# Kernel optimization log

Hardware: AMD Instinct MI355X
Metric: run time of the kernel (lower is better)

Reference implementation:

```python
import jax, jax.numpy as jnp
import numpy as np

DEPTH = 11          # tree depth
D = 1024            # input_width
H = 32              # hidden_width (leaf MLP)
O = 1024            # output_width
B = 4096            # flattened token batch
N_LEAVES = 2 ** DEPTH
N_NODES = 2 ** DEPTH - 1


def setup_inputs() -> dict:
    key = jax.random.key(0)
    ks = jax.random.split(key, 7)
    f1 = 1.0 / np.sqrt(D)
    f2 = 1.0 / np.sqrt(H)
    u = lambda k, shape, f: jax.random.uniform(k, shape, jnp.float32, -f, f)
    return {
        "x": jax.random.normal(ks[0], (B, D), jnp.float32),
        "node_weights": u(ks[1], (N_NODES, D), f1),
        "node_biases": u(ks[2], (N_NODES,), f1),   # (n_nodes,1) in torch; flattened
        "w1s": u(ks[3], (N_LEAVES, D, H), f1),
        "b1s": u(ks[4], (N_LEAVES, H), f1),
        "w2s": u(ks[5], (N_LEAVES, H, O), f2),
        "b2s": u(ks[6], (N_LEAVES, O), f2),
    }


def reference(x, node_weights, node_biases, w1s, b1s, w2s, b2s):
    # --- hard tree descent (eval_forward) ---
    nodes = jnp.zeros((x.shape[0],), jnp.int32)
    for i in range(DEPTH):  # fixed small loop over tree depth
        w = node_weights[nodes]                       # [B, D] gathered plane coeffs
        b = node_biases[nodes]                        # [B]
        score = jnp.einsum('bd,bd->b', x, w) + b      # per-sample dot product
        choice = (score >= 0).astype(jnp.int32)
        platform = 2 ** i - 1
        next_platform = 2 ** (i + 1) - 1
        nodes = (nodes - platform) * 2 + choice + next_platform
    leaves = nodes - (2 ** DEPTH - 1)                 # [B] leaf index per sample

    # --- per-sample leaf MLP with gathered weights ---
    h = jax.nn.relu(jnp.einsum('bd,bdh->bh', x, w1s[leaves]) + b1s[leaves])  # [B, H]
    out = jnp.einsum('bh,bho->bo', h, w2s[leaves]) + b2s[leaves]             # [B, O]
    return out
```

## Files before the change

kernel.cpp:

```cpp
#include <hip/hip_runtime.h>

#define DEPTH 11
#define D 1024
#define H 32
#define OW 1024
#define B 4096
#define N_LEAVES 2048
#define N_NODES 2047
#define SMAX 4
#define MAX_ITEMS 3072

typedef __attribute__((address_space(3))) void lds_void;
typedef const __attribute__((address_space(1))) void glb_void;

#define WAITV8  do { asm volatile("s_waitcnt vmcnt(8)" ::: "memory"); __builtin_amdgcn_sched_barrier(0); } while (0)
#define WAITV4  do { asm volatile("s_waitcnt vmcnt(4)" ::: "memory"); __builtin_amdgcn_sched_barrier(0); } while (0)
#define WAITV0  do { asm volatile("s_waitcnt vmcnt(0)" ::: "memory"); __builtin_amdgcn_sched_barrier(0); } while (0)
#define WAITLG0 do { asm volatile("s_waitcnt lgkmcnt(0)" ::: "memory"); __builtin_amdgcn_sched_barrier(0); } while (0)

__global__ __launch_bounds__(256) void descent_kernel(
    const float* __restrict__ x, const float* __restrict__ nw,
    const float* __restrict__ nb, int* __restrict__ leaf,
    int* __restrict__ rnk, int* __restrict__ count)
{
    int lane = threadIdx.x & 63;
    int wv   = threadIdx.x >> 6;
    int samp = blockIdx.x * 4 + wv;

    const float4* xp = (const float4*)(x + (size_t)samp * D);
    float4 xf[4];
#pragma unroll
    for (int k = 0; k < 4; k++) xf[k] = xp[lane + 64 * k];

    int node = 0;
#pragma unroll
    for (int i = 0; i < DEPTH; i++) {
        const float4* wp = (const float4*)(nw + (size_t)node * D);
        double s = 0.0;
#pragma unroll
        for (int k = 0; k < 4; k++) {
            float4 wf = wp[lane + 64 * k];
            s += (double)xf[k].x * (double)wf.x;
            s += (double)xf[k].y * (double)wf.y;
            s += (double)xf[k].z * (double)wf.z;
            s += (double)xf[k].w * (double)wf.w;
        }
#pragma unroll
        for (int m = 32; m >= 1; m >>= 1) s += __shfl_xor(s, m, 64);
        double score = s + (double)nb[node];
        int choice = (score >= 0.0) ? 1 : 0;
        node = 2 * node + 1 + choice;
    }
    int lf = node - N_NODES;
    if (lane == 0) {
        leaf[samp] = lf;
        rnk[samp]  = atomicAdd(&count[lf], 1);
    }
}

__global__ __launch_bounds__(256) void scan_kernel(
    const int* __restrict__ count, int* __restrict__ offsets)
{
    __shared__ int tot[256];
    int t = threadIdx.x;
    int c[8], s = 0;
#pragma unroll
    for (int k = 0; k < 8; k++) { c[k] = count[t * 8 + k]; s += c[k]; }
    tot[t] = s;
    __syncthreads();
    for (int off = 1; off < 256; off <<= 1) {
        int v = (t >= off) ? tot[t - off] : 0;
        __syncthreads();
        tot[t] += v;
        __syncthreads();
    }
    int base = (t > 0) ? tot[t - 1] : 0;
#pragma unroll
    for (int k = 0; k < 8; k++) { offsets[t * 8 + k] = base; base += c[k]; }
}

__global__ __launch_bounds__(256) void scatter_kernel(
    const int* __restrict__ leaf, const int* __restrict__ rnk,
    const int* __restrict__ offsets, int* __restrict__ bucket)
{
    int i = blockIdx.x * 256 + threadIdx.x;
    bucket[offsets[leaf[i]] + rnk[i]] = i;
}

__global__ __launch_bounds__(256) void build_items_kernel(
    const int* __restrict__ count, int* __restrict__ items,
    int* __restrict__ nitems)
{
    int l = blockIdx.x * 256 + threadIdx.x;
    int c = count[l];
    if (c > 0) {
        int k = (c + SMAX - 1) / SMAX;
        int base = atomicAdd(nitems, k);
        for (int i = 0; i < k; i++)
            items[base + i] = l | ((i * SMAX) << 11);
    }
}

__device__ __forceinline__ void stage4k(const float* src, float* dst, int lane)
{
#pragma unroll
    for (int i = 0; i < 4; i++)
        __builtin_amdgcn_global_load_lds((glb_void*)(src + i * 256 + lane * 4),
                                         (lds_void*)(dst + i * 256), 16, 0, 0);
}

__device__ __forceinline__ void stageL2(const float* w2w, int cj, float* dst, int lane)
{
#pragma unroll
    for (int jl = 0; jl < 4; jl++)
        __builtin_amdgcn_global_load_lds(
            (glb_void*)(w2w + (size_t)(cj * 4 + jl) * OW + lane * 4),
            (lds_void*)(dst + jl * 256), 16, 0, 0);
}

template <int SS>
__device__ __forceinline__ void l1c(const float* p, const float* xsw, int c,
                                    int lane, int dg, float4* acc)
{
#pragma unroll
    for (int u = 0; u < 4; u++) {
        float4 w = ((const float4*)p)[u * 64 + lane];
#pragma unroll
        for (int s = 0; s < SS; s++) {
            float xv = xsw[s * D + c * 32 + u * 8 + dg];
            acc[s].x += xv * w.x;
            acc[s].y += xv * w.y;
            acc[s].z += xv * w.z;
            acc[s].w += xv * w.w;
        }
    }
}

template <int SS>
__device__ __forceinline__ void l2c(const float* p, const float (*hs)[H], int cj,
                                    int lane, float4* o)
{
#pragma unroll
    for (int jl = 0; jl < 4; jl++) {
        float4 w = ((const float4*)p)[jl * 64 + lane];
#pragma unroll
        for (int s = 0; s < SS; s++) {
            float hv = hs[s][cj * 4 + jl];
            o[s].x += hv * w.x;
            o[s].y += hv * w.y;
            o[s].z += hv * w.z;
            o[s].w += hv * w.w;
        }
    }
}

template <int SS>
__device__ __forceinline__ void mlp_item(
    int tid, const float* __restrict__ x, const float* __restrict__ w1,
    const float* __restrict__ w2, const float* __restrict__ b1,
    const float* __restrict__ b2, const int* __restrict__ bucket, int base,
    float* xs, float* wq, float (*pl1)[SMAX][32], float (*hs)[H],
    float* __restrict__ out)
{
    const int lane = tid & 63, wave = tid >> 6;
    const int jq = lane & 7, dg = lane >> 3;

    float b1v = b1[tid & 31];
    asm volatile("" :: "v"(b1v));

    int sid[SS];
#pragma unroll
    for (int s = 0; s < SS; s++) sid[s] = bucket[base + s];

#pragma unroll
    for (int s = 0; s < SS; s++)
        __builtin_amdgcn_global_load_lds(
            (glb_void*)(x + (size_t)sid[s] * D + wave * 256 + lane * 4),
            (lds_void*)(xs + s * D + wave * 256), 16, 0, 0);

    const float* w1w = w1 + wave * 8192;
    const float* xsw = xs + wave * 256;
    stage4k(w1w + 0 * 1024, wq + 0 * 1024, lane);
    stage4k(w1w + 1 * 1024, wq + 1 * 1024, lane);
    stage4k(w1w + 2 * 1024, wq + 2 * 1024, lane);

    float4 acc[SS];
#pragma unroll
    for (int s = 0; s < SS; s++) acc[s] = make_float4(0.f, 0.f, 0.f, 0.f);

    WAITV8; l1c<SS>(wq + 0 * 1024, xsw, 0, lane, dg, acc); stage4k(w1w + 3 * 1024, wq + 0 * 1024, lane);
    WAITV8; l1c<SS>(wq + 1 * 1024, xsw, 1, lane, dg, acc); stage4k(w1w + 4 * 1024, wq + 1 * 1024, lane);
    WAITV8; l1c<SS>(wq + 2 * 1024, xsw, 2, lane, dg, acc); stage4k(w1w + 5 * 1024, wq + 2 * 1024, lane);
    WAITV8; l1c<SS>(wq + 0 * 1024, xsw, 3, lane, dg, acc); stage4k(w1w + 6 * 1024, wq + 0 * 1024, lane);
    WAITV8; l1c<SS>(wq + 1 * 1024, xsw, 4, lane, dg, acc); stage4k(w1w + 7 * 1024, wq + 1 * 1024, lane);
    WAITV8; l1c<SS>(wq + 2 * 1024, xsw, 5, lane, dg, acc);
    WAITV4; l1c<SS>(wq + 0 * 1024, xsw, 6, lane, dg, acc);
    WAITV0; l1c<SS>(wq + 1 * 1024, xsw, 7, lane, dg, acc);

#pragma unroll
    for (int m = 8; m <= 32; m <<= 1)
#pragma unroll
        for (int s = 0; s < SS; s++) {
            acc[s].x += __shfl_xor(acc[s].x, m, 64);
            acc[s].y += __shfl_xor(acc[s].y, m, 64);
            acc[s].z += __shfl_xor(acc[s].z, m, 64);
            acc[s].w += __shfl_xor(acc[s].w, m, 64);
        }
    if (dg == 0) {
#pragma unroll
        for (int s = 0; s < SS; s++)
            *(float4*)&pl1[wave][s][jq * 4] = acc[s];
    }

    const float* w2w = w2 + wave * 256;
    stageL2(w2w, 0, wq + 0 * 1024, lane);
    stageL2(w2w, 1, wq + 1 * 1024, lane);
    stageL2(w2w, 2, wq + 2 * 1024, lane);

    WAITLG0;
    __builtin_amdgcn_s_barrier();
    if (tid < 32 * SS) {
        int s2 = tid >> 5, j2 = tid & 31;
        float sum = pl1[0][s2][j2] + pl1[1][s2][j2] + pl1[2][s2][j2] +
                    pl1[3][s2][j2] + b1v;
        hs[s2][j2] = fmaxf(sum, 0.f);
    }
    WAITLG0;
    __builtin_amdgcn_s_barrier();

    float4 o[SS];
#pragma unroll
    for (int s = 0; s < SS; s++) o[s] = make_float4(0.f, 0.f, 0.f, 0.f);

    WAITV8; l2c<SS>(wq + 0 * 1024, hs, 0, lane, o); stageL2(w2w, 3, wq + 0 * 1024, lane);
    WAITV8; l2c<SS>(wq + 1 * 1024, hs, 1, lane, o); stageL2(w2w, 4, wq + 1 * 1024, lane);
    WAITV8; l2c<SS>(wq + 2 * 1024, hs, 2, lane, o); stageL2(w2w, 5, wq + 2 * 1024, lane);
    WAITV8; l2c<SS>(wq + 0 * 1024, hs, 3, lane, o); stageL2(w2w, 6, wq + 0 * 1024, lane);
    WAITV8; l2c<SS>(wq + 1 * 1024, hs, 4, lane, o); stageL2(w2w, 7, wq + 1 * 1024, lane);
    WAITV8; l2c<SS>(wq + 2 * 1024, hs, 5, lane, o);
    WAITV4; l2c<SS>(wq + 0 * 1024, hs, 6, lane, o);
    WAITV0; l2c<SS>(wq + 1 * 1024, hs, 7, lane, o);

    float4 bv = *(const float4*)(b2 + wave * 256 + lane * 4);
#pragma unroll
    for (int s = 0; s < SS; s++) {
        float4 o4;
        o4.x = o[s].x + bv.x;
        o4.y = o[s].y + bv.y;
        o4.z = o[s].z + bv.z;
        o4.w = o[s].w + bv.w;
        *(float4*)(out + (size_t)sid[s] * OW + wave * 256 + lane * 4) = o4;
    }
}

__global__ __launch_bounds__(256, 2) void mlp_kernel(
    const float* __restrict__ x, const float* __restrict__ w1s,
    const float* __restrict__ b1s, const float* __restrict__ w2s,
    const float* __restrict__ b2s, const int* __restrict__ offsets,
    const int* __restrict__ count, const int* __restrict__ bucket,
    const int* __restrict__ items, const int* __restrict__ nitems,
    float* __restrict__ out)
{
    __shared__ float xs[SMAX * D];
    __shared__ float wbuf[4 * 3 * 1024];
    __shared__ float pl1[4][SMAX][32];
    __shared__ float hs[SMAX][H];

    if ((int)blockIdx.x >= nitems[0]) return;
    int item  = items[blockIdx.x];
    int l     = item & (N_LEAVES - 1);
    int start = item >> 11;
    int S     = min(SMAX, count[l] - start);
    int base  = offsets[l] + start;
    int tid   = threadIdx.x;

    const float* w1 = w1s + (size_t)l * D * H;
    const float* w2 = w2s + (size_t)l * H * OW;
    const float* b1 = b1s + (size_t)l * H;
    const float* b2 = b2s + (size_t)l * OW;
    float* wq = wbuf + (tid >> 6) * 3 * 1024;

    switch (S) {
        case 1: mlp_item<1>(tid, x, w1, w2, b1, b2, bucket, base, xs, wq, pl1, hs, out); break;
        case 2: mlp_item<2>(tid, x, w1, w2, b1, b2, bucket, base, xs, wq, pl1, hs, out); break;
        case 3: mlp_item<3>(tid, x, w1, w2, b1, b2, bucket, base, xs, wq, pl1, hs, out); break;
        default: mlp_item<4>(tid, x, w1, w2, b1, b2, bucket, base, xs, wq, pl1, hs, out); break;
    }
}

extern "C" void kernel_launch(void* const* d_in, const int* in_sizes, int n_in,
                              void* d_out, int out_size, void* d_ws, size_t ws_size,
                              hipStream_t stream)
{
    const float* x   = (const float*)d_in[0];
    const float* nw  = (const float*)d_in[1];
    const float* nb  = (const float*)d_in[2];
    const float* w1s = (const float*)d_in[3];
    const float* b1s = (const float*)d_in[4];
    const float* w2s = (const float*)d_in[5];
    const float* b2s = (const float*)d_in[6];
    float* out = (float*)d_out;

    int* leaf    = (int*)d_ws;
    int* rnk     = leaf + B;
    int* count   = rnk + B;
    int* offsets = count + N_LEAVES;
    int* bucket  = offsets + N_LEAVES;
    int* items   = bucket + B;
    int* nitems  = items + MAX_ITEMS;

    hipMemsetAsync(count, 0, N_LEAVES * sizeof(int), stream);
    hipMemsetAsync(nitems, 0, sizeof(int), stream);
    descent_kernel<<<B / 4, 256, 0, stream>>>(x, nw, nb, leaf, rnk, count);
    scan_kernel<<<1, 256, 0, stream>>>(count, offsets);
    scatter_kernel<<<B / 256, 256, 0, stream>>>(leaf, rnk, offsets, bucket);
    build_items_kernel<<<N_LEAVES / 256, 256, 0, stream>>>(count, items, nitems);
    mlp_kernel<<<MAX_ITEMS, 256, 0, stream>>>(x, w1s, b1s, w2s, b2s,
                                              offsets, count, bucket,
                                              items, nitems, out);
}
```

Before: 125.9 us.

## Make MLP kernel persistent with cross-item weight prefetch and double buffering

Replaces the one-block-per-item launch with a fixed grid of 512 blocks. Each block loops over up to six work items, with item metadata loaded into shared memory up front. While the layer-2 tail of the current leaf runs, the block prefetches the next leaf's first W1 tiles, input rows and biases, so load latency overlaps between items. The staging buffer shrinks from triple to double buffering. The per-size template specialization is dropped: every item is computed as four samples, padded by repeating the last sample id, which wastes some compute and redundantly stores outputs for small items. The prologue also issues one duplicated W1 stage.

After: 129.8 us. 3.1% more time.

```diff
diff --git a/kernel.cpp b/kernel.cpp
--- a/kernel.cpp
+++ b/kernel.cpp
@@ -9,14 +9,17 @@
 #define N_NODES 2047
 #define SMAX 4
 #define MAX_ITEMS 3072
+#define NBLK 512
+#define MAXK 6
 
 typedef __attribute__((address_space(3))) void lds_void;
 typedef const __attribute__((address_space(1))) void glb_void;
 
-#define WAITV8  do { asm volatile("s_waitcnt vmcnt(8)" ::: "memory"); __builtin_amdgcn_sched_barrier(0); } while (0)
-#define WAITV4  do { asm volatile("s_waitcnt vmcnt(4)" ::: "memory"); __builtin_amdgcn_sched_barrier(0); } while (0)
-#define WAITV0  do { asm volatile("s_waitcnt vmcnt(0)" ::: "memory"); __builtin_amdgcn_sched_barrier(0); } while (0)
-#define WAITLG0 do { asm volatile("s_waitcnt lgkmcnt(0)" ::: "memory"); __builtin_amdgcn_sched_barrier(0); } while (0)
+#define SB __builtin_amdgcn_sched_barrier(0)
+#define WAITV(N) do { asm volatile("s_waitcnt vmcnt(" #N ")" ::: "memory"); SB; } while (0)
+#define WAITLG0  do { asm volatile("s_waitcnt lgkmcnt(0)" ::: "memory"); SB; } while (0)
+#define BARRIER  do { WAITLG0; __builtin_amdgcn_s_barrier(); \
+                      asm volatile("" ::: "memory"); SB; } while (0)
 
 __global__ __launch_bounds__(256) void descent_kernel(
     const float* __restrict__ x, const float* __restrict__ nw,
@@ -101,7 +104,7 @@
     }
 }
 
-__device__ __forceinline__ void stage4k(const float* src, float* dst, int lane)
+__device__ __forceinline__ void stage4(const float* src, float* dst, int lane)
 {
 #pragma unroll
     for (int i = 0; i < 4; i++)
@@ -109,7 +112,7 @@
                                          (lds_void*)(dst + i * 256), 16, 0, 0);
 }
 
-__device__ __forceinline__ void stageL2(const float* w2w, int cj, float* dst, int lane)
+__device__ __forceinline__ void stageL2g(const float* w2w, int cj, float* dst, int lane)
 {
 #pragma unroll
     for (int jl = 0; jl < 4; jl++)
@@ -118,7 +121,22 @@
             (lds_void*)(dst + jl * 256), 16, 0, 0);
 }
 
-template <int SS>
+__device__ __forceinline__ void stageXB(const float* x, const int* sid4,
+                                        const float* b1, const float* b2,
+                                        float* xsd, float* b1d, float* b2d,
+                                        int wave, int lane)
+{
+#pragma unroll
+    for (int s = 0; s < 4; s++)
+        __builtin_amdgcn_global_load_lds(
+            (glb_void*)(x + (size_t)sid4[s] * D + wave * 256 + lane * 4),
+            (lds_void*)(xsd + s * D + wave * 256), 16, 0, 0);
+    __builtin_amdgcn_global_load_lds(
+        (glb_void*)(b1 + ((lane < 32) ? lane : 31)), (lds_void*)b1d, 4, 0, 0);
+    __builtin_amdgcn_global_load_lds(
+        (glb_void*)(b2 + wave * 256 + lane * 4), (lds_void*)b2d, 16, 0, 0);
+}
+
 __device__ __forceinline__ void l1c(const float* p, const float* xsw, int c,
                                     int lane, int dg, float4* acc)
 {
@@ -126,7 +144,7 @@
     for (int u = 0; u < 4; u++) {
         float4 w = ((const float4*)p)[u * 64 + lane];
 #pragma unroll
-        for (int s = 0; s < SS; s++) {
+        for (int s = 0; s < 4; s++) {
             float xv = xsw[s * D + c * 32 + u * 8 + dg];
             acc[s].x += xv * w.x;
             acc[s].y += xv * w.y;
@@ -136,120 +154,20 @@
     }
 }
 
-template <int SS>
-__device__ __forceinline__ void l2c(const float* p, const float (*hs)[H], int cj,
+__device__ __forceinline__ void l2c(const float* p, const float (*hsv)[32], int cj,
                                     int lane, float4* o)
 {
 #pragma unroll
     for (int jl = 0; jl < 4; jl++) {
         float4 w = ((const float4*)p)[jl * 64 + lane];
 #pragma unroll
-        for (int s = 0; s < SS; s++) {
-            float hv = hs[s][cj * 4 + jl];
+        for (int s = 0; s < 4; s++) {
+            float hv = hsv[s][cj * 4 + jl];
             o[s].x += hv * w.x;
             o[s].y += hv * w.y;
             o[s].z += hv * w.z;
             o[s].w += hv * w.w;
         }
-    }
-}
-
-template <int SS>
-__device__ __forceinline__ void mlp_item(
-    int tid, const float* __restrict__ x, const float* __restrict__ w1,
-    const float* __restrict__ w2, const float* __restrict__ b1,
-    const float* __restrict__ b2, const int* __restrict__ bucket, int base,
-    float* xs, float* wq, float (*pl1)[SMAX][32], float (*hs)[H],
-    float* __restrict__ out)
-{
-    const int lane = tid & 63, wave = tid >> 6;
-    const int jq = lane & 7, dg = lane >> 3;
-
-    float b1v = b1[tid & 31];
-    asm volatile("" :: "v"(b1v));
-
-    int sid[SS];
-#pragma unroll
-    for (int s = 0; s < SS; s++) sid[s] = bucket[base + s];
-
-#pragma unroll
-    for (int s = 0; s < SS; s++)
-        __builtin_amdgcn_global_load_lds(
-            (glb_void*)(x + (size_t)sid[s] * D + wave * 256 + lane * 4),
-            (lds_void*)(xs + s * D + wave * 256), 16, 0, 0);
-
-    const float* w1w = w1 + wave * 8192;
-    const float* xsw = xs + wave * 256;
-    stage4k(w1w + 0 * 1024, wq + 0 * 1024, lane);
-    stage4k(w1w + 1 * 1024, wq + 1 * 1024, lane);
-    stage4k(w1w + 2 * 1024, wq + 2 * 1024, lane);
-
-    float4 acc[SS];
-#pragma unroll
-    for (int s = 0; s < SS; s++) acc[s] = make_float4(0.f, 0.f, 0.f, 0.f);
-
-    WAITV8; l1c<SS>(wq + 0 * 1024, xsw, 0, lane, dg, acc); stage4k(w1w + 3 * 1024, wq + 0 * 1024, lane);
-    WAITV8; l1c<SS>(wq + 1 * 1024, xsw, 1, lane, dg, acc); stage4k(w1w + 4 * 1024, wq + 1 * 1024, lane);
-    WAITV8; l1c<SS>(wq + 2 * 1024, xsw, 2, lane, dg, acc); stage4k(w1w + 5 * 1024, wq + 2 * 1024, lane);
-    WAITV8; l1c<SS>(wq + 0 * 1024, xsw, 3, lane, dg, acc); stage4k(w1w + 6 * 1024, wq + 0 * 1024, lane);
-    WAITV8; l1c<SS>(wq + 1 * 1024, xsw, 4, lane, dg, acc); stage4k(w1w + 7 * 1024, wq + 1 * 1024, lane);
-    WAITV8; l1c<SS>(wq + 2 * 1024, xsw, 5, lane, dg, acc);
-    WAITV4; l1c<SS>(wq + 0 * 1024, xsw, 6, lane, dg, acc);
-    WAITV0; l1c<SS>(wq + 1 * 1024, xsw, 7, lane, dg, acc);
-
-#pragma unroll
-    for (int m = 8; m <= 32; m <<= 1)
-#pragma unroll
-        for (int s = 0; s < SS; s++) {
-            acc[s].x += __shfl_xor(acc[s].x, m, 64);
-            acc[s].y += __shfl_xor(acc[s].y, m, 64);
-            acc[s].z += __shfl_xor(acc[s].z, m, 64);
-            acc[s].w += __shfl_xor(acc[s].w, m, 64);
-        }
-    if (dg == 0) {
-#pragma unroll
-        for (int s = 0; s < SS; s++)
-            *(float4*)&pl1[wave][s][jq * 4] = acc[s];
-    }
-
-    const float* w2w = w2 + wave * 256;
-    stageL2(w2w, 0, wq + 0 * 1024, lane);
-    stageL2(w2w, 1, wq + 1 * 1024, lane);
-    stageL2(w2w, 2, wq + 2 * 1024, lane);
-
-    WAITLG0;
-    __builtin_amdgcn_s_barrier();
-    if (tid < 32 * SS) {
-        int s2 = tid >> 5, j2 = tid & 31;
-        float sum = pl1[0][s2][j2] + pl1[1][s2][j2] + pl1[2][s2][j2] +
-                    pl1[3][s2][j2] + b1v;
-        hs[s2][j2] = fmaxf(sum, 0.f);
-    }
-    WAITLG0;
-    __builtin_amdgcn_s_barrier();
-
-    float4 o[SS];
-#pragma unroll
-    for (int s = 0; s < SS; s++) o[s] = make_float4(0.f, 0.f, 0.f, 0.f);
-
-    WAITV8; l2c<SS>(wq + 0 * 1024, hs, 0, lane, o); stageL2(w2w, 3, wq + 0 * 1024, lane);
-    WAITV8; l2c<SS>(wq + 1 * 1024, hs, 1, lane, o); stageL2(w2w, 4, wq + 1 * 1024, lane);
-    WAITV8; l2c<SS>(wq + 2 * 1024, hs, 2, lane, o); stageL2(w2w, 5, wq + 2 * 1024, lane);
-    WAITV8; l2c<SS>(wq + 0 * 1024, hs, 3, lane, o); stageL2(w2w, 6, wq + 0 * 1024, lane);
-    WAITV8; l2c<SS>(wq + 1 * 1024, hs, 4, lane, o); stageL2(w2w, 7, wq + 1 * 1024, lane);
-    WAITV8; l2c<SS>(wq + 2 * 1024, hs, 5, lane, o);
-    WAITV4; l2c<SS>(wq + 0 * 1024, hs, 6, lane, o);
-    WAITV0; l2c<SS>(wq + 1 * 1024, hs, 7, lane, o);
-
-    float4 bv = *(const float4*)(b2 + wave * 256 + lane * 4);
-#pragma unroll
-    for (int s = 0; s < SS; s++) {
-        float4 o4;
-        o4.x = o[s].x + bv.x;
-        o4.y = o[s].y + bv.y;
-        o4.z = o[s].z + bv.z;
-        o4.w = o[s].w + bv.w;
-        *(float4*)(out + (size_t)sid[s] * OW + wave * 256 + lane * 4) = o4;
     }
 }
 
@@ -262,29 +180,126 @@
     float* __restrict__ out)
 {
     __shared__ float xs[SMAX * D];
-    __shared__ float wbuf[4 * 3 * 1024];
+    __shared__ float wq_[4][2][1024];
     __shared__ float pl1[4][SMAX][32];
-    __shared__ float hs[SMAX][H];
-
-    if ((int)blockIdx.x >= nitems[0]) return;
-    int item  = items[blockIdx.x];
-    int l     = item & (N_LEAVES - 1);
-    int start = item >> 11;
-    int S     = min(SMAX, count[l] - start);
-    int base  = offsets[l] + start;
-    int tid   = threadIdx.x;
-
-    const float* w1 = w1s + (size_t)l * D * H;
-    const float* w2 = w2s + (size_t)l * H * OW;
-    const float* b1 = b1s + (size_t)l * H;
-    const float* b2 = b2s + (size_t)l * OW;
-    float* wq = wbuf + (tid >> 6) * 3 * 1024;
-
-    switch (S) {
-        case 1: mlp_item<1>(tid, x, w1, w2, b1, b2, bucket, base, xs, wq, pl1, hs, out); break;
-        case 2: mlp_item<2>(tid, x, w1, w2, b1, b2, bucket, base, xs, wq, pl1, hs, out); break;
-        case 3: mlp_item<3>(tid, x, w1, w2, b1, b2, bucket, base, xs, wq, pl1, hs, out); break;
-        default: mlp_item<4>(tid, x, w1, w2, b1, b2, bucket, base, xs, wq, pl1, hs, out); break;
+    __shared__ float hs[SMAX][32];
+    __shared__ float b1l[2][4][64];
+    __shared__ float b2l[2][4][256];
+    __shared__ int   md_leaf[MAXK];
+    __shared__ int   md_sid[MAXK][4];
+
+    const int tid = threadIdx.x, lane = tid & 63, wave = tid >> 6;
+    const int dg = lane >> 3;
+    const int bid = blockIdx.x;
+
+    int nit = nitems[0];
+    if (tid < MAXK) {
+        int idx = bid + tid * NBLK;
+        if (idx < nit) {
+            int it = items[idx];
+            int l = it & (N_LEAVES - 1), st = it >> 11;
+            int c = count[l] - st;
+            int S = (c < SMAX) ? c : SMAX;
+            int off = offsets[l] + st;
+            md_leaf[tid] = l;
+            for (int s = 0; s < 4; s++)
+                md_sid[tid][s] = bucket[off + ((s < S) ? s : (S - 1))];
+        }
+    }
+    __syncthreads();
+    int n_my = (nit - bid + NBLK - 1) >> 9;
+    if (n_my <= 0) return;
+    if (n_my > MAXK) n_my = MAXK;
+
+    float* WQ0 = &wq_[wave][0][0];
+    float* WQ1 = &wq_[wave][1][0];
+    const float* xsw = xs + wave * 256;
+
+    int lc = md_leaf[0];
+    {
+        const float* w1w = w1s + (size_t)lc * 32768 + wave * 8192;
+        stage4(w1w, WQ0, lane);
+        stageXB(x, md_sid[0], b1s + lc * H, b2s + (size_t)lc * OW,
+                xs, &b1l[0][wave][0], &b2l[0][wave][0], wave, lane);
+        stage4(w1w + 1024, WQ1, lane);
+        stage4(w1w + 1024, WQ1, lane);
+    }
+
+    for (int k = 0; k < n_my; k++) {
+        const int p  = k & 1;
+        const int kn = (k + 1 < n_my) ? (k + 1) : k;
+        const int ln = md_leaf[kn];
+        const float* w1c = w1s + (size_t)lc * 32768 + wave * 8192;
+        const float* w2c = w2s + (size_t)lc * 32768 + wave * 256;
+        const float* w1n = w1s + (size_t)ln * 32768 + wave * 8192;
+        int sc[4];
+#pragma unroll
+        for (int s = 0; s < 4; s++) sc[s] = md_sid[k][s];
+
+        float4 acc[4];
+#pragma unroll
+        for (int s = 0; s < 4; s++) acc[s] = make_float4(0.f, 0.f, 0.f, 0.f);
+
+        WAITV(8);  l1c(WQ0, xsw, 0, lane, dg, acc); SB; stage4(w1c + 2 * 1024, WQ0, lane);
+        WAITV(8);  l1c(WQ1, xsw, 1, lane, dg, acc); SB; stage4(w1c + 3 * 1024, WQ1, lane);
+        WAITV(4);  l1c(WQ0, xsw, 2, lane, dg, acc); SB; stage4(w1c + 4 * 1024, WQ0, lane);
+        WAITV(4);  l1c(WQ1, xsw, 3, lane, dg, acc); SB; stage4(w1c + 5 * 1024, WQ1, lane);
+        WAITV(4);  l1c(WQ0, xsw, 4, lane, dg, acc); SB; stage4(w1c + 6 * 1024, WQ0, lane);
+        WAITV(4);  l1c(WQ1, xsw, 5, lane, dg, acc); SB; stage4(w1c + 7 * 1024, WQ1, lane);
+        WAITV(4);  l1c(WQ0, xsw, 6, lane, dg, acc); SB; stageL2g(w2c, 0, WQ0, lane);
+        WAITV(4);  l1c(WQ1, xsw, 7, lane, dg, acc); SB; stageL2g(w2c, 1, WQ1, lane);
+
+#pragma unroll
+        for (int m = 8; m <= 32; m <<= 1)
+#pragma unroll
+            for (int s = 0; s < 4; s++) {
+                acc[s].x += __shfl_xor(acc[s].x, m, 64);
+                acc[s].y += __shfl_xor(acc[s].y, m, 64);
+                acc[s].z += __shfl_xor(acc[s].z, m, 64);
+                acc[s].w += __shfl_xor(acc[s].w, m, 64);
+            }
+        if (dg == 0) {
+#pragma unroll
+            for (int s = 0; s < 4; s++)
+                *(float4*)&pl1[wave][s][(lane & 7) * 4] = acc[s];
+        }
+        BARRIER;
+        if (tid < 128) {
+            int s2 = tid >> 5, j2 = tid & 31;
+            float sum = pl1[0][s2][j2] + pl1[1][s2][j2] + pl1[2][s2][j2] +
+                        pl1[3][s2][j2] + b1l[p][tid >> 6][j2];
+            hs[s2][j2] = fmaxf(sum, 0.f);
+        }
+        BARRIER;
+
+        float4 o[4];
+#pragma unroll
+        for (int s = 0; s < 4; s++) o[s] = make_float4(0.f, 0.f, 0.f, 0.f);
+
+        WAITV(4);  l2c(WQ0, hs, 0, lane, o); SB; stageL2g(w2c, 2, WQ0, lane);
+        WAITV(4);  l2c(WQ1, hs, 1, lane, o); SB; stageL2g(w2c, 3, WQ1, lane);
+        WAITV(4);  l2c(WQ0, hs, 2, lane, o); SB; stageL2g(w2c, 4, WQ0, lane);
+        WAITV(4);  l2c(WQ1, hs, 3, lane, o); SB; stageL2g(w2c, 5, WQ1, lane);
+        WAITV(4);  l2c(WQ0, hs, 4, lane, o); SB; stageL2g(w2c, 6, WQ0, lane);
+        WAITV(4);  l2c(WQ1, hs, 5, lane, o); SB; stageL2g(w2c, 7, WQ1, lane);
+        WAITV(4);  l2c(WQ0, hs, 6, lane, o); SB;
+        stage4(w1n, WQ0, lane);
+        stageXB(x, md_sid[kn], b1s + ln * H, b2s + (size_t)ln * OW,
+                xs, &b1l[p ^ 1][wave][0], &b2l[p ^ 1][wave][0], wave, lane);
+        WAITV(10); l2c(WQ1, hs, 7, lane, o); SB;
+        stage4(w1n + 1024, WQ1, lane);
+
+        float4 bv = ((const float4*)&b2l[p][wave][0])[lane];
+#pragma unroll
+        for (int s = 0; s < 4; s++) {
+            float4 o4;
+            o4.x = o[s].x + bv.x;
+            o4.y = o[s].y + bv.y;
+            o4.z = o[s].z + bv.z;
+            o4.w = o[s].w + bv.w;
+            *(float4*)(out + (size_t)sc[s] * OW + wave * 256 + lane * 4) = o4;
+        }
+        lc = ln;
     }
 }
 
@@ -315,7 +330,7 @@
     scan_kernel<<<1, 256, 0, stream>>>(count, offsets);
     scatter_kernel<<<B / 256, 256, 0, stream>>>(leaf, rnk, offsets, bucket);
     build_items_kernel<<<N_LEAVES / 256, 256, 0, stream>>>(count, items, nitems);
-    mlp_kernel<<<MAX_ITEMS, 256, 0, stream>>>(x, w1s, b1s, w2s, b2s,
-                                              offsets, count, bucket,
-                                              items, nitems, out);
-}
+    mlp_kernel<<<NBLK, 256, 0, stream>>>(x, w1s, b1s, w2s, b2s,
+                                         offsets, count, bucket,
+                                         items, nitems, out);
+}
```
